# Optimization experiments

Measured on AMD Instinct MI355X. Metric: run time of the kernel, lower is better.

## Reference

```python
import jax, jax.numpy as jnp
import numpy as np

MAX_AGENTS = 64
IN_DIM = 256
HID_DIM = 512
OUT_DIM = 256
MAX_CHILDREN = 8
BATCH = 1024


def setup_inputs() -> dict:
    key = jax.random.key(0)
    k1, k2, k3, k4, k5 = jax.random.split(key, 5)
    W1 = jax.random.normal(k1, (MAX_AGENTS, IN_DIM, HID_DIM), dtype=jnp.float32) * 0.02
    b1 = jnp.zeros((MAX_AGENTS, HID_DIM), dtype=jnp.float32)
    W2 = jax.random.normal(k2, (MAX_AGENTS, HID_DIM, OUT_DIM), dtype=jnp.float32) * 0.02
    b2 = jnp.zeros((MAX_AGENTS, OUT_DIM), dtype=jnp.float32)
    router_weights = jax.random.normal(k3, (MAX_AGENTS, HID_DIM, MAX_CHILDREN), dtype=jnp.float32) * 0.01
    agent_indices = jax.random.randint(k4, (BATCH,), 0, MAX_AGENTS, dtype=jnp.int64 if jax.config.jax_enable_x64 else jnp.int32)
    x = jax.random.normal(k5, (BATCH, IN_DIM), dtype=jnp.float32)
    return {
        "x": x,
        "W1": W1,
        "b1": b1,
        "W2": W2,
        "b2": b2,
        "router_weights": router_weights,
        "agent_indices": agent_indices,
    }


def reference(x, W1, b1, W2, b2, router_weights, agent_indices):
    # Gather per-sample weights (same as torch advanced indexing W1[agent_indices])
    w1 = W1[agent_indices]           # [B, In, Hid]
    b1g = b1[agent_indices]          # [B, Hid]
    w2 = W2[agent_indices]           # [B, Hid, Out]
    b2g = b2[agent_indices]          # [B, Out]
    rw = router_weights[agent_indices]  # [B, Hid, C]

    # per-sample MLP: bmm with a singleton row -> einsum
    h = jax.nn.relu(jnp.einsum('bi,bih->bh', x, w1) + b1g)      # [B, Hid]
    out = jnp.einsum('bh,bho->bo', h, w2) + b2g                 # [B, Out]
    r_logits = jnp.einsum('bh,bhc->bc', h, rw)                  # [B, C]
    return (h, out, r_logits)
```

## Files before the change

### kernel.cpp

```cpp
#include <hip/hip_runtime.h>

#define IN_DIM   256
#define HID_DIM  512
#define OUT_DIM  256
#define N_CHILD  8
#define BATCH    1024

#define SB    16
#define XPAD  20
#define MAXCH 128

__device__ __forceinline__ int sort_chunk(const int* __restrict__ raw, const int c,
                                          int* s_cnt, int* s_info, int* s_wsum,
                                          int* s_sid)
{
    const int t = threadIdx.x;
    const int lane = t & 63, w = t >> 6;
    if (t < 64) s_cnt[t] = 0;
    if (t == 0) { s_info[2] = 0; s_info[3] = 0; }
    __syncthreads();
    if (raw[2 * t + 1] != 0 || raw[2 * (t + 256) + 1] != 0) s_info[3] = 1;
    __syncthreads();
    const int is32 = s_info[3];
    int myid[4];
    #pragma unroll
    for (int j = 0; j < 4; ++j) {
        const int i = t * 4 + j;
        const int v = (is32 ? raw[i] : raw[2 * i]) & 63;
        myid[j] = v;
        atomicAdd(&s_cnt[v], 1);
    }
    __syncthreads();
    if (t < 64) {
        const int ca  = s_cnt[t];
        const int nch = (ca + SB - 1) / SB;
        int sn = nch;
        #pragma unroll
        for (int d = 1; d < 64; d <<= 1) {
            const int v = __shfl_up(sn, d);
            if (lane >= d) sn += v;
        }
        const int chb = sn - nch;
        if (c >= chb && c < chb + nch) {
            s_info[0] = t;
            const int p = (c - chb) * SB;
            s_info[1] = p;
            s_info[2] = (ca - p < SB) ? (ca - p) : SB;
        }
    }
    __syncthreads();
    const int len = s_info[2];
    if (len == 0) return 0;
    const int a = s_info[0], p = s_info[1];
    int m = 0;
    #pragma unroll
    for (int j = 0; j < 4; ++j) if (myid[j] == a) ++m;
    int inc = m;
    #pragma unroll
    for (int d = 1; d < 64; d <<= 1) {
        const int v = __shfl_up(inc, d);
        if (lane >= d) inc += v;
    }
    if (lane == 63) s_wsum[w] = inc;
    __syncthreads();
    int base = inc - m;
    #pragma unroll
    for (int ww = 0; ww < 4; ++ww) if (ww < w) base += s_wsum[ww];
    #pragma unroll
    for (int j = 0; j < 4; ++j)
        if (myid[j] == a) {
            const int r = (base++) - p;
            if (r >= 0 && r < SB) s_sid[r] = t * 4 + j;
        }
    __syncthreads();
    if (t >= len && t < SB) s_sid[t] = s_sid[len - 1];
    __syncthreads();
    return len;
}

extern "C" __global__ __launch_bounds__(256, 4)
void k1_mlp1(const float* __restrict__ x, const float* __restrict__ W1,
             const float* __restrict__ b1, const float* __restrict__ rw,
             const int* __restrict__ raw,
             float* __restrict__ h_out, float* __restrict__ r_part)
{
    __shared__ float xT[IN_DIM * XPAD];
    __shared__ int s_cnt[64], s_info[4], s_wsum[4], s_sid[SB];

    const int c = blockIdx.x;
    const int t = threadIdx.x;
    const int len = sort_chunk(raw, c, s_cnt, s_info, s_wsum, s_sid);
    if (len == 0) return;
    const int a = s_info[0];
    const int bcol = blockIdx.y * 64;

    #pragma unroll
    for (int s = 0; s < SB; ++s)
        xT[t * XPAD + s] = x[(size_t)s_sid[s] * IN_DIM + t];
    __syncthreads();

    const int cg = t & 15;
    const int kq = (t >> 4) & 3;
    const int w  = t >> 6;
    if (w * 4 >= len) return;

    const float* Wb = W1 + (size_t)a * IN_DIM * HID_DIM + bcol + cg * 4;

    float acc[16];
    #pragma unroll
    for (int i = 0; i < 16; ++i) acc[i] = 0.f;

    #pragma unroll
    for (int i = 0; i < 64; ++i) {
        const int row = i * 4 + kq;
        const float4 wv = *(const float4*)(Wb + (size_t)row * HID_DIM);
        const float4 xv = *(const float4*)(&xT[row * XPAD + w * 4]);
        const float wa[4] = {wv.x, wv.y, wv.z, wv.w};
        const float xa[4] = {xv.x, xv.y, xv.z, xv.w};
        #pragma unroll
        for (int cc = 0; cc < 4; ++cc)
            #pragma unroll
            for (int s = 0; s < 4; ++s)
                acc[cc * 4 + s] = fmaf(wa[cc], xa[s], acc[cc * 4 + s]);
    }

    #pragma unroll
    for (int i = 0; i < 16; ++i) {
        acc[i] += __shfl_xor(acc[i], 16);
        acc[i] += __shfl_xor(acc[i], 32);
    }
    if (kq != 0) return;

    const float4 bv = *(const float4*)(b1 + a * HID_DIM + bcol + cg * 4);
    const float ba[4] = {bv.x, bv.y, bv.z, bv.w};
    float hv[16];
    #pragma unroll
    for (int cc = 0; cc < 4; ++cc)
        #pragma unroll
        for (int s = 0; s < 4; ++s)
            hv[cc * 4 + s] = fmaxf(acc[cc * 4 + s] + ba[cc], 0.f);

    #pragma unroll
    for (int s = 0; s < 4; ++s) {
        float4 v = make_float4(hv[0 * 4 + s], hv[1 * 4 + s],
                               hv[2 * 4 + s], hv[3 * 4 + s]);
        *(float4*)(h_out + (size_t)s_sid[w * 4 + s] * HID_DIM + bcol + cg * 4) = v;
    }

    float rp[32];
    #pragma unroll
    for (int i = 0; i < 32; ++i) rp[i] = 0.f;
    const float* rwa = rw + (size_t)a * HID_DIM * N_CHILD
                          + (size_t)(bcol + cg * 4) * N_CHILD;
    #pragma unroll
    for (int j = 0; j < 4; ++j)
        #pragma unroll
        for (int ch = 0; ch < 8; ++ch) {
            const float rv = rwa[j * N_CHILD + ch];
            #pragma unroll
            for (int s = 0; s < 4; ++s)
                rp[s * 8 + ch] = fmaf(hv[j * 4 + s], rv, rp[s * 8 + ch]);
        }
    #pragma unroll
    for (int i = 0; i < 32; ++i) {
        rp[i] += __shfl_xor(rp[i], 1);
        rp[i] += __shfl_xor(rp[i], 2);
        rp[i] += __shfl_xor(rp[i], 4);
        rp[i] += __shfl_xor(rp[i], 8);
    }
    if (cg == 0) {
        float* rb = r_part + ((size_t)c * 8 + blockIdx.y) * 128 + w * 32;
        #pragma unroll
        for (int s4 = 0; s4 < 8; ++s4)
            *(float4*)(rb + s4 * 4) = make_float4(rp[s4*4+0], rp[s4*4+1],
                                                  rp[s4*4+2], rp[s4*4+3]);
    }
}

extern "C" __global__ __launch_bounds__(256, 4)
void k2_mlp2(const float* __restrict__ h, const float* __restrict__ W2,
             const float* __restrict__ b2, const int* __restrict__ raw,
             const float* __restrict__ r_part,
             float* __restrict__ o_out, float* __restrict__ r_out)
{
    __shared__ float hT[256 * XPAD];
    __shared__ int s_cnt[64], s_info[4], s_wsum[4], s_sid[SB];

    const int c = blockIdx.x;
    const int t = threadIdx.x;
    const int len = sort_chunk(raw, c, s_cnt, s_info, s_wsum, s_sid);
    if (len == 0) return;
    const int a = s_info[0];
    const int bcol = blockIdx.y * 32;

    const int cg = t & 7;
    const int kq = (t >> 3) & 7;
    const int w  = t >> 6;
    const bool act = (w * 4) < len;
    const float* Wb = W2 + (size_t)a * HID_DIM * OUT_DIM + bcol + cg * 4;

    float acc[16];
    #pragma unroll
    for (int i = 0; i < 16; ++i) acc[i] = 0.f;

    #pragma unroll
    for (int half = 0; half < 2; ++half) {
        const int kb = half * 256;
        #pragma unroll
        for (int s = 0; s < SB; ++s)
            hT[t * XPAD + s] = h[(size_t)s_sid[s] * HID_DIM + kb + t];
        __syncthreads();
        if (act) {
            #pragma unroll
            for (int i = 0; i < 32; ++i) {
                const int row = i * 8 + kq;
                const float4 wv = *(const float4*)(Wb + (size_t)(kb + row) * OUT_DIM);
                const float4 xv = *(const float4*)(&hT[row * XPAD + w * 4]);
                const float wa[4] = {wv.x, wv.y, wv.z, wv.w};
                const float xa[4] = {xv.x, xv.y, xv.z, xv.w};
                #pragma unroll
                for (int cc = 0; cc < 4; ++cc)
                    #pragma unroll
                    for (int s = 0; s < 4; ++s)
                        acc[cc * 4 + s] = fmaf(wa[cc], xa[s], acc[cc * 4 + s]);
            }
        }
        if (half == 0) __syncthreads();
    }

    if (act) {
        #pragma unroll
        for (int i = 0; i < 16; ++i) {
            acc[i] += __shfl_xor(acc[i], 8);
            acc[i] += __shfl_xor(acc[i], 16);
            acc[i] += __shfl_xor(acc[i], 32);
        }
        if (kq == 0) {
            const float4 bv = *(const float4*)(b2 + a * OUT_DIM + bcol + cg * 4);
            #pragma unroll
            for (int s = 0; s < 4; ++s) {
                const int g = w * 4 + s;
                if (g < len) {
                    float4 v = make_float4(acc[0*4+s] + bv.x, acc[1*4+s] + bv.y,
                                           acc[2*4+s] + bv.z, acc[3*4+s] + bv.w);
                    *(float4*)(o_out + (size_t)s_sid[g] * OUT_DIM + bcol + cg * 4) = v;
                }
            }
        }
    }
    if (blockIdx.y == 0 && t < 128) {
        const int s = t >> 3;
        if (s < len) {
            float sum = 0.f;
            #pragma unroll
            for (int yy = 0; yy < 8; ++yy)
                sum += r_part[((size_t)c * 8 + yy) * 128 + t];
            r_out[(size_t)s_sid[s] * N_CHILD + (t & 7)] = sum;
        }
    }
}

extern "C" void kernel_launch(void* const* d_in, const int* in_sizes, int n_in,
                              void* d_out, int out_size, void* d_ws, size_t ws_size,
                              hipStream_t stream) {
    const float* x  = (const float*)d_in[0];
    const float* W1 = (const float*)d_in[1];
    const float* b1 = (const float*)d_in[2];
    const float* W2 = (const float*)d_in[3];
    const float* b2 = (const float*)d_in[4];
    const float* rw = (const float*)d_in[5];
    const int* raw  = (const int*)d_in[6];

    float* r_part = (float*)d_ws;

    float* out   = (float*)d_out;
    float* h_out = out;
    float* o_out = h_out + (size_t)BATCH * HID_DIM;
    float* r_out = o_out + (size_t)BATCH * OUT_DIM;

    hipLaunchKernelGGL(k1_mlp1, dim3(MAXCH, 8), dim3(256), 0, stream,
                       x, W1, b1, rw, raw, h_out, r_part);
    hipLaunchKernelGGL(k2_mlp2, dim3(MAXCH, 8), dim3(256), 0, stream,
                       h_out, W2, b2, raw, r_part, o_out, r_out);
}
```

Measured before the change: 145.1 us.

## Stage weight tiles through double-buffered LDS with register prefetch in both MLP kernels

Both MLP kernels now cooperatively load weight tiles (and, in the second kernel, h tiles) into double-buffered shared memory, prefetching the next tile into registers while computing on the current one. Previously each thread streamed weights directly from global memory in its inner loop. The aim is to overlap global loads with FMA work and to coalesce weight loads across all threads, including the inactive warps of partial chunks. In exchange it uses more LDS, which may limit occupancy, and adds a barrier every tile.

```diff
diff --git a/kernel.cpp b/kernel.cpp
--- a/kernel.cpp
+++ b/kernel.cpp
@@ -85,6 +85,7 @@
              float* __restrict__ h_out, float* __restrict__ r_part)
 {
     __shared__ float xT[IN_DIM * XPAD];
+    __shared__ float wS[2][32 * 64];
     __shared__ int s_cnt[64], s_info[4], s_wsum[4], s_sid[SB];
 
     const int c = blockIdx.x;
@@ -94,128 +95,39 @@
     const int a = s_info[0];
     const int bcol = blockIdx.y * 64;
 
-    #pragma unroll
-    for (int s = 0; s < SB; ++s)
-        xT[t * XPAD + s] = x[(size_t)s_sid[s] * IN_DIM + t];
-    __syncthreads();
-
     const int cg = t & 15;
     const int kq = (t >> 4) & 3;
     const int w  = t >> 6;
-    if (w * 4 >= len) return;
-
-    const float* Wb = W1 + (size_t)a * IN_DIM * HID_DIM + bcol + cg * 4;
+    const bool act = (w * 4) < len;
+    const int row0 = t >> 4;
+    const int sc4  = (t & 15) * 4;
+
+    const float* Wb = W1 + (size_t)a * IN_DIM * HID_DIM + bcol;
+    #define WLD(P,I) (*(const float4*)(Wb + (size_t)((P)*32 + row0 + (I)*16) * HID_DIM + sc4))
+
+    float4 ldA0 = WLD(0,0), ldA1 = WLD(0,1);
+
+    #pragma unroll
+    for (int s = 0; s < SB; ++s)
+        xT[t * XPAD + s] = x[(size_t)s_sid[s] * IN_DIM + t];
 
     float acc[16];
     #pragma unroll
     for (int i = 0; i < 16; ++i) acc[i] = 0.f;
 
-    #pragma unroll
-    for (int i = 0; i < 64; ++i) {
-        const int row = i * 4 + kq;
-        const float4 wv = *(const float4*)(Wb + (size_t)row * HID_DIM);
-        const float4 xv = *(const float4*)(&xT[row * XPAD + w * 4]);
-        const float wa[4] = {wv.x, wv.y, wv.z, wv.w};
-        const float xa[4] = {xv.x, xv.y, xv.z, xv.w};
-        #pragma unroll
-        for (int cc = 0; cc < 4; ++cc)
-            #pragma unroll
-            for (int s = 0; s < 4; ++s)
-                acc[cc * 4 + s] = fmaf(wa[cc], xa[s], acc[cc * 4 + s]);
-    }
-
-    #pragma unroll
-    for (int i = 0; i < 16; ++i) {
-        acc[i] += __shfl_xor(acc[i], 16);
-        acc[i] += __shfl_xor(acc[i], 32);
-    }
-    if (kq != 0) return;
-
-    const float4 bv = *(const float4*)(b1 + a * HID_DIM + bcol + cg * 4);
-    const float ba[4] = {bv.x, bv.y, bv.z, bv.w};
-    float hv[16];
-    #pragma unroll
-    for (int cc = 0; cc < 4; ++cc)
-        #pragma unroll
-        for (int s = 0; s < 4; ++s)
-            hv[cc * 4 + s] = fmaxf(acc[cc * 4 + s] + ba[cc], 0.f);
-
-    #pragma unroll
-    for (int s = 0; s < 4; ++s) {
-        float4 v = make_float4(hv[0 * 4 + s], hv[1 * 4 + s],
-                               hv[2 * 4 + s], hv[3 * 4 + s]);
-        *(float4*)(h_out + (size_t)s_sid[w * 4 + s] * HID_DIM + bcol + cg * 4) = v;
-    }
-
-    float rp[32];
-    #pragma unroll
-    for (int i = 0; i < 32; ++i) rp[i] = 0.f;
-    const float* rwa = rw + (size_t)a * HID_DIM * N_CHILD
-                          + (size_t)(bcol + cg * 4) * N_CHILD;
-    #pragma unroll
-    for (int j = 0; j < 4; ++j)
-        #pragma unroll
-        for (int ch = 0; ch < 8; ++ch) {
-            const float rv = rwa[j * N_CHILD + ch];
-            #pragma unroll
-            for (int s = 0; s < 4; ++s)
-                rp[s * 8 + ch] = fmaf(hv[j * 4 + s], rv, rp[s * 8 + ch]);
-        }
-    #pragma unroll
-    for (int i = 0; i < 32; ++i) {
-        rp[i] += __shfl_xor(rp[i], 1);
-        rp[i] += __shfl_xor(rp[i], 2);
-        rp[i] += __shfl_xor(rp[i], 4);
-        rp[i] += __shfl_xor(rp[i], 8);
-    }
-    if (cg == 0) {
-        float* rb = r_part + ((size_t)c * 8 + blockIdx.y) * 128 + w * 32;
-        #pragma unroll
-        for (int s4 = 0; s4 < 8; ++s4)
-            *(float4*)(rb + s4 * 4) = make_float4(rp[s4*4+0], rp[s4*4+1],
-                                                  rp[s4*4+2], rp[s4*4+3]);
-    }
-}
-
-extern "C" __global__ __launch_bounds__(256, 4)
-void k2_mlp2(const float* __restrict__ h, const float* __restrict__ W2,
-             const float* __restrict__ b2, const int* __restrict__ raw,
-             const float* __restrict__ r_part,
-             float* __restrict__ o_out, float* __restrict__ r_out)
-{
-    __shared__ float hT[256 * XPAD];
-    __shared__ int s_cnt[64], s_info[4], s_wsum[4], s_sid[SB];
-
-    const int c = blockIdx.x;
-    const int t = threadIdx.x;
-    const int len = sort_chunk(raw, c, s_cnt, s_info, s_wsum, s_sid);
-    if (len == 0) return;
-    const int a = s_info[0];
-    const int bcol = blockIdx.y * 32;
-
-    const int cg = t & 7;
-    const int kq = (t >> 3) & 7;
-    const int w  = t >> 6;
-    const bool act = (w * 4) < len;
-    const float* Wb = W2 + (size_t)a * HID_DIM * OUT_DIM + bcol + cg * 4;
-
-    float acc[16];
-    #pragma unroll
-    for (int i = 0; i < 16; ++i) acc[i] = 0.f;
-
-    #pragma unroll
-    for (int half = 0; half < 2; ++half) {
-        const int kb = half * 256;
-        #pragma unroll
-        for (int s = 0; s < SB; ++s)
-            hT[t * XPAD + s] = h[(size_t)s_sid[s] * HID_DIM + kb + t];
+    for (int p = 0; p < 8; ++p) {
+        float4 ldB0 = ldA0, ldB1 = ldA1;
+        if (p < 7) { ldB0 = WLD(p+1,0); ldB1 = WLD(p+1,1); }
+        float* buf = wS[p & 1];
+        *(float4*)(&buf[(row0 +  0) * 64 + sc4]) = ldA0;
+        *(float4*)(&buf[(row0 + 16) * 64 + sc4]) = ldA1;
         __syncthreads();
         if (act) {
             #pragma unroll
-            for (int i = 0; i < 32; ++i) {
-                const int row = i * 8 + kq;
-                const float4 wv = *(const float4*)(Wb + (size_t)(kb + row) * OUT_DIM);
-                const float4 xv = *(const float4*)(&hT[row * XPAD + w * 4]);
+            for (int i = 0; i < 8; ++i) {
+                const int row = i * 4 + kq;
+                const float4 wv = *(const float4*)(&buf[row * 64 + cg * 4]);
+                const float4 xv = *(const float4*)(&xT[(p * 32 + row) * XPAD + w * 4]);
                 const float wa[4] = {wv.x, wv.y, wv.z, wv.w};
                 const float xa[4] = {xv.x, xv.y, xv.z, xv.w};
                 #pragma unroll
@@ -225,8 +137,137 @@
                         acc[cc * 4 + s] = fmaf(wa[cc], xa[s], acc[cc * 4 + s]);
             }
         }
-        if (half == 0) __syncthreads();
-    }
+        ldA0 = ldB0; ldA1 = ldB1;
+    }
+    #undef WLD
+
+    if (!act) return;
+    #pragma unroll
+    for (int i = 0; i < 16; ++i) {
+        acc[i] += __shfl_xor(acc[i], 16);
+        acc[i] += __shfl_xor(acc[i], 32);
+    }
+    if (kq != 0) return;
+
+    const float4 bv = *(const float4*)(b1 + a * HID_DIM + bcol + cg * 4);
+    const float ba[4] = {bv.x, bv.y, bv.z, bv.w};
+    float hv[16];
+    #pragma unroll
+    for (int cc = 0; cc < 4; ++cc)
+        #pragma unroll
+        for (int s = 0; s < 4; ++s)
+            hv[cc * 4 + s] = fmaxf(acc[cc * 4 + s] + ba[cc], 0.f);
+
+    #pragma unroll
+    for (int s = 0; s < 4; ++s) {
+        float4 v = make_float4(hv[0 * 4 + s], hv[1 * 4 + s],
+                               hv[2 * 4 + s], hv[3 * 4 + s]);
+        *(float4*)(h_out + (size_t)s_sid[w * 4 + s] * HID_DIM + bcol + cg * 4) = v;
+    }
+
+    float rp[32];
+    #pragma unroll
+    for (int i = 0; i < 32; ++i) rp[i] = 0.f;
+    const float* rwa = rw + (size_t)a * HID_DIM * N_CHILD
+                          + (size_t)(bcol + cg * 4) * N_CHILD;
+    #pragma unroll
+    for (int j = 0; j < 4; ++j)
+        #pragma unroll
+        for (int ch = 0; ch < 8; ++ch) {
+            const float rv = rwa[j * N_CHILD + ch];
+            #pragma unroll
+            for (int s = 0; s < 4; ++s)
+                rp[s * 8 + ch] = fmaf(hv[j * 4 + s], rv, rp[s * 8 + ch]);
+        }
+    #pragma unroll
+    for (int i = 0; i < 32; ++i) {
+        rp[i] += __shfl_xor(rp[i], 1);
+        rp[i] += __shfl_xor(rp[i], 2);
+        rp[i] += __shfl_xor(rp[i], 4);
+        rp[i] += __shfl_xor(rp[i], 8);
+    }
+    if (cg == 0) {
+        float* rb = r_part + ((size_t)c * 8 + blockIdx.y) * 128 + w * 32;
+        #pragma unroll
+        for (int s4 = 0; s4 < 8; ++s4)
+            *(float4*)(rb + s4 * 4) = make_float4(rp[s4*4+0], rp[s4*4+1],
+                                                  rp[s4*4+2], rp[s4*4+3]);
+    }
+}
+
+extern "C" __global__ __launch_bounds__(256, 4)
+void k2_mlp2(const float* __restrict__ h, const float* __restrict__ W2,
+             const float* __restrict__ b2, const int* __restrict__ raw,
+             const float* __restrict__ r_part,
+             float* __restrict__ o_out, float* __restrict__ r_out)
+{
+    __shared__ float hT[2][64 * XPAD];
+    __shared__ float wS[2][64 * 32];
+    __shared__ int s_cnt[64], s_info[4], s_wsum[4], s_sid[SB];
+
+    const int c = blockIdx.x;
+    const int t = threadIdx.x;
+    const int len = sort_chunk(raw, c, s_cnt, s_info, s_wsum, s_sid);
+    if (len == 0) return;
+    const int a = s_info[0];
+    const int bcol = blockIdx.y * 32;
+
+    const int cg = t & 7;
+    const int kq = (t >> 3) & 7;
+    const int w  = t >> 6;
+    const bool act = (w * 4) < len;
+    const int row0 = t >> 3;
+    const int sc4  = (t & 7) * 4;
+    const int hrow = t & 63;
+    const int hsb  = (t >> 6) * 4;
+
+    const float* Wb = W2 + (size_t)a * HID_DIM * OUT_DIM + bcol;
+    #define WLD2(P,I) (*(const float4*)(Wb + (size_t)((P)*64 + row0 + (I)*32) * OUT_DIM + sc4))
+    #define HLD(P,J)  (h[(size_t)s_sid[hsb + (J)] * HID_DIM + (P)*64 + hrow])
+
+    float4 wA0 = WLD2(0,0), wA1 = WLD2(0,1);
+    float  hA0 = HLD(0,0),  hA1 = HLD(0,1),  hA2 = HLD(0,2),  hA3 = HLD(0,3);
+
+    float acc[16];
+    #pragma unroll
+    for (int i = 0; i < 16; ++i) acc[i] = 0.f;
+
+    for (int p = 0; p < 8; ++p) {
+        float4 wB0 = wA0, wB1 = wA1;
+        float  hB0 = hA0, hB1 = hA1, hB2 = hA2, hB3 = hA3;
+        if (p < 7) {
+            wB0 = WLD2(p+1,0); wB1 = WLD2(p+1,1);
+            hB0 = HLD(p+1,0);  hB1 = HLD(p+1,1);
+            hB2 = HLD(p+1,2);  hB3 = HLD(p+1,3);
+        }
+        const int b = p & 1;
+        hT[b][hrow * XPAD + hsb + 0] = hA0;
+        hT[b][hrow * XPAD + hsb + 1] = hA1;
+        hT[b][hrow * XPAD + hsb + 2] = hA2;
+        hT[b][hrow * XPAD + hsb + 3] = hA3;
+        *(float4*)(&wS[b][(row0 +  0) * 32 + sc4]) = wA0;
+        *(float4*)(&wS[b][(row0 + 32) * 32 + sc4]) = wA1;
+        __syncthreads();
+        if (act) {
+            #pragma unroll
+            for (int i = 0; i < 8; ++i) {
+                const int row = i * 8 + kq;
+                const float4 wv = *(const float4*)(&wS[b][row * 32 + cg * 4]);
+                const float4 xv = *(const float4*)(&hT[b][row * XPAD + w * 4]);
+                const float wa[4] = {wv.x, wv.y, wv.z, wv.w};
+                const float xa[4] = {xv.x, xv.y, xv.z, xv.w};
+                #pragma unroll
+                for (int cc = 0; cc < 4; ++cc)
+                    #pragma unroll
+                    for (int s = 0; s < 4; ++s)
+                        acc[cc * 4 + s] = fmaf(wa[cc], xa[s], acc[cc * 4 + s]);
+            }
+        }
+        wA0 = wB0; wA1 = wB1;
+        hA0 = hB0; hA1 = hB1; hA2 = hB2; hA3 = hB3;
+    }
+    #undef WLD2
+    #undef HLD
 
     if (act) {
         #pragma unroll
```

Result: faster. 136.8 us (-5.7%).
